# Performance work log

Measured on AMD Instinct MI355X. Metric: run time of the kernel, lower is better.

The kernel has to match this reference:

```python
import jax, jax.numpy as jnp
import numpy as np

B, T, LEAF, A = 128, 50, 4880, 64
INTERNAL = 728
ATTN = 128   # attn_dim_size (GRU input)
RNN = 128    # rnn_dim_size
G = 128      # g_dim_size (== RNN, required by broadcast in forward)
NC = 283     # num_class
VERY_NEG = -1e30


def setup_inputs() -> dict:
    key = jax.random.key(0)
    ks = jax.random.split(key, 16)
    s = 0.05
    inputs_x = jax.random.uniform(ks[0], (B, T, LEAF), jnp.float32)
    inputs_f = jax.random.randint(ks[1], (B, T, A), 0, INTERNAL + 1)  # 0 = padding
    mask_seqs = jnp.ones((B, T), jnp.float32)
    dag_emb = jax.random.normal(ks[2], (LEAF, ATTN), jnp.float32) * s
    embed_a = jax.random.normal(ks[3], (INTERNAL + 1, G), jnp.float32) * s
    embed_a = embed_a.at[0].set(0.0)  # padding row
    # 2-layer GRU params (torch layout: [3H, in], gates r,z,n)
    Wih0 = jax.random.normal(ks[4], (3 * RNN, ATTN), jnp.float32) * s
    Whh0 = jax.random.normal(ks[5], (3 * RNN, RNN), jnp.float32) * s
    bih0 = jax.random.normal(ks[6], (3 * RNN,), jnp.float32) * s
    bhh0 = jax.random.normal(ks[7], (3 * RNN,), jnp.float32) * s
    Wih1 = jax.random.normal(ks[8], (3 * RNN, RNN), jnp.float32) * s
    Whh1 = jax.random.normal(ks[9], (3 * RNN, RNN), jnp.float32) * s
    bih1 = jax.random.normal(ks[10], (3 * RNN,), jnp.float32) * s
    bhh1 = jax.random.normal(ks[11], (3 * RNN,), jnp.float32) * s
    fc_w = jax.random.normal(ks[12], (NC, 2 * RNN), jnp.float32) * s
    fc_b = jax.random.normal(ks[13], (NC,), jnp.float32) * s
    return dict(inputs_x=inputs_x, inputs_f=inputs_f, mask_seqs=mask_seqs,
                dag_emb=dag_emb, embed_a=embed_a,
                Wih0=Wih0, Whh0=Whh0, bih0=bih0, bhh0=bhh0,
                Wih1=Wih1, Whh1=Whh1, bih1=bih1, bhh1=bhh1,
                fc_w=fc_w, fc_b=fc_b)


def _gru_layer(x, Wih, Whh, bih, bhh):
    # x: [B, T, I] -> out [B, T, H]; h0 = zeros
    H = Whh.shape[1]
    xW = jnp.einsum('bti,gi->btg', x, Wih) + bih  # [B,T,3H], precompute input gates
    h0 = jnp.zeros((x.shape[0], H), x.dtype)

    def step(h, xw_t):  # xw_t: [B,3H]
        gh = h @ Whh.T + bhh
        xr, xz, xn = jnp.split(xw_t, 3, axis=-1)
        hr, hz, hn = jnp.split(gh, 3, axis=-1)
        r = jax.nn.sigmoid(xr + hr)
        z = jax.nn.sigmoid(xz + hz)
        n = jnp.tanh(xn + r * hn)
        h_new = (1.0 - z) * n + z * h
        return h_new, h_new

    _, ys = jax.lax.scan(step, h0, jnp.swapaxes(xW, 0, 1))  # scan over T
    return jnp.swapaxes(ys, 0, 1)


def reference(inputs_x, inputs_f, mask_seqs, dag_emb, embed_a,
              Wih0, Whh0, bih0, bhh0, Wih1, Whh1, bih1, bhh1, fc_w, fc_b):
    # x = tanh(inputs_x @ dag_emb): [B,T,ATTN]
    x = jnp.tanh(jnp.einsum('btl,la->bta', inputs_x, dag_emb))
    # 2-layer GRU (no dropout at inference)
    h1 = _gru_layer(x, Wih0, Whh0, bih0, bhh0)
    out = _gru_layer(h1, Wih1, Whh1, bih1, bhh1)  # [B,T,RNN]
    # gather ancestor embeddings: [B,T,A,G]
    l = embed_a[inputs_f]
    # masked dot-product attention over ancestors
    hl = jnp.einsum('bth,btah->bta', out, l)
    mask_ans = inputs_f > 0
    hl = hl + jnp.where(mask_ans, 0.0, VERY_NEG)
    weights = jax.nn.softmax(hl, axis=-1)  # [B,T,A]
    k = jnp.einsum('bta,btah->bth', weights, l)
    s = jnp.concatenate([out, k], axis=-1)  # [B,T,2*RNN]
    output = jax.nn.sigmoid(s @ fc_w.T + fc_b)
    return output * mask_seqs[:, :, None]
```

## Files before the change

kernel.cpp:

```cpp
#include <hip/hip_runtime.h>
#include <math.h>

#define B_DIM 128
#define T_DIM 50
#define LEAF  4880
#define A_DIM 64
#define ATTN  128
#define RNN   128
#define NC    283
#define M_TOT (B_DIM*T_DIM)
#define KSPLIT 10
#define NCH 153
#define WT_PLANE (NCH*512*8)

using short8 = __attribute__((ext_vector_type(8))) short;
using short4v = __attribute__((ext_vector_type(4))) short;
using f32x4  = __attribute__((ext_vector_type(4))) float;

__device__ __forceinline__ float sigmoidf_(float x) {
  return 1.0f / (1.0f + __expf(-x));
}

__device__ __forceinline__ unsigned short f32_to_bf16_rne(float f) {
  unsigned int u = __float_as_uint(f);
  unsigned int r = u + 0x7FFFu + ((u >> 16) & 1u);
  return (unsigned short)(r >> 16);
}
__device__ __forceinline__ float bf16_bits_to_f32(unsigned short b) {
  return __uint_as_float(((unsigned int)b) << 16);
}

__global__ __launch_bounds__(256) void k_prep(
    const float* __restrict__ Wd,
    const float* __restrict__ Wih0, const float* __restrict__ Wih1,
    const float* __restrict__ fcw,
    unsigned short* __restrict__ Wt,
    unsigned short* __restrict__ Bt0, unsigned short* __restrict__ Bt1,
    unsigned short* __restrict__ Bt2) {
  const int bx = blockIdx.x;
  const int tid = threadIdx.x;
  if (bx < 306) {
    const int u = bx * 256 + tid;
    const int c = u >> 9, rem = u & 511;
    const int nt = rem >> 6, lane = rem & 63;
    const int n = nt * 16 + (lane & 15);
    const int kb = c * 32 + ((lane >> 4) << 3);
    short8 h8, l8;
    #pragma unroll
    for (int j = 0; j < 8; ++j) {
      int k = kb + j;
      float v = (k < LEAF) ? Wd[(size_t)k * 128 + n] : 0.0f;
      unsigned short hb = f32_to_bf16_rne(v);
      unsigned short lb = f32_to_bf16_rne(v - bf16_bits_to_f32(hb));
      h8[j] = (short)hb;
      l8[j] = (short)lb;
    }
    *(short8*)&Wt[(size_t)u * 8] = h8;
    *(short8*)&Wt[(size_t)WT_PLANE + (size_t)u * 8] = l8;
  } else {
    const float* src; unsigned short* dst; int N, K, s0;
    if (bx < 330)      { src = Wih0; dst = Bt0; N = 384; K = 128; s0 = (bx - 306) * 256; }
    else if (bx < 354) { src = Wih1; dst = Bt1; N = 384; K = 128; s0 = (bx - 330) * 256; }
    else               { src = fcw;  dst = Bt2; N = NC;  K = 256; s0 = (bx - 354) * 256; }
    const int s = s0 + tid;
    const int PL = (K / 32) * 24 * 512;
    const int kc = s / (24 * 64);
    const int r  = s % (24 * 64);
    const int nt = r >> 6, lane = r & 63;
    const int n  = nt * 16 + (lane & 15);
    const int kb = kc * 32 + ((lane >> 4) << 3);
    short8 h8, l8;
    #pragma unroll
    for (int j = 0; j < 8; ++j) {
      float v = (n < N) ? src[(size_t)n * K + kb + j] : 0.0f;
      unsigned short hb = f32_to_bf16_rne(v);
      unsigned short lb = f32_to_bf16_rne(v - bf16_bits_to_f32(hb));
      h8[j] = (short)hb;
      l8[j] = (short)lb;
    }
    *(short8*)&dst[(size_t)s * 8] = h8;
    *(short8*)&dst[(size_t)PL + (size_t)s * 8] = l8;
  }
}

__global__ __launch_bounds__(512, 4) void k_gemm_mfma(
    const float* __restrict__ Ax, const unsigned short* __restrict__ Wt,
    float* __restrict__ P) {
  __shared__ __align__(16) unsigned short As[2][8192];
  const int tid  = threadIdx.x;
  const int lane = tid & 63;
  const int w    = tid >> 6;
  const int M0   = blockIdx.x * 128;
  const int s    = blockIdx.y;
  const int c0   = (s * NCH) / KSPLIT;
  const int c1   = ((s + 1) * NCH) / KSPLIT;

  const int am = tid >> 2;
  const int kq = tid & 3;
  const float* pA = Ax + (size_t)(M0 + am) * LEAF;
  const int a_idx = (am >> 4) * 512 + ((am & 15) + 16 * kq) * 8;

  f32x4 acc[8];
  #pragma unroll
  for (int i = 0; i < 8; ++i) {
    #pragma unroll
    for (int q = 0; q < 4; ++q) acc[i][q] = 0.0f;
  }

  float4 rA_a0, rA_a1, rA_b0, rA_b1;
  short8 bh_a, bl_a, bh_b, bl_b;

  auto issueB = [&](int c, short8& bh, short8& bl) {
    const size_t o = ((size_t)c * 512 + w * 64 + lane) * 8;
    bh = *(const short8*)&Wt[o];
    bl = *(const short8*)&Wt[(size_t)WT_PLANE + o];
  };
  auto issueA = [&](int c, float4& r0, float4& r1) {
    int kk = c * 32 + kq * 8;
    kk = min(kk, LEAF - 8);
    r0 = *(const float4*)(pA + kk);
    r1 = *(const float4*)(pA + kk + 4);
  };
  auto storeA = [&](int p, float4 r0, float4 r1) {
    float v[8] = {r0.x, r0.y, r0.z, r0.w, r1.x, r1.y, r1.z, r1.w};
    short8 h8, l8;
    #pragma unroll
    for (int j = 0; j < 8; ++j) {
      unsigned short hb = f32_to_bf16_rne(v[j]);
      unsigned short lb = f32_to_bf16_rne(v[j] - bf16_bits_to_f32(hb));
      h8[j] = (short)hb;
      l8[j] = (short)lb;
    }
    *(short8*)&As[p][a_idx] = h8;
    *(short8*)&As[p][4096 + a_idx] = l8;
  };
  auto compute = [&](int p, const short8& bh, const short8& bl) {
    #pragma unroll
    for (int m = 0; m < 8; ++m) {
      short8 a_hi = *(const short8*)&As[p][m * 512 + lane * 8];
      short8 a_lo = *(const short8*)&As[p][4096 + m * 512 + lane * 8];
      acc[m] = __builtin_amdgcn_mfma_f32_16x16x32_bf16(a_hi, bl, acc[m], 0, 0, 0);
      acc[m] = __builtin_amdgcn_mfma_f32_16x16x32_bf16(a_lo, bh, acc[m], 0, 0, 0);
      acc[m] = __builtin_amdgcn_mfma_f32_16x16x32_bf16(a_hi, bh, acc[m], 0, 0, 0);
    }
  };

  {
    float4 t0, t1;
    issueA(c0, t0, t1);
    asm volatile("s_waitcnt vmcnt(0)" ::: "memory");
    storeA(0, t0, t1);
    issueB(c0, bh_a, bl_a);
    asm volatile("" ::: "memory");
    if (c0 + 1 < c1) issueA(c0 + 1, rA_a0, rA_a1);
    asm volatile("s_waitcnt lgkmcnt(0)" ::: "memory");
    __builtin_amdgcn_s_barrier();
    asm volatile("" ::: "memory");
  }

#define GEMM_ITER(BHc, BLc, BHn, BLn, RAc0, RAc1, RAn0, RAn1)                 \
  {                                                                           \
    const int p = (c - c0) & 1;                                               \
    const bool has1 = (c + 1 < c1), has2 = (c + 2 < c1);                      \
    if (has1) { issueB(c + 1, BHn, BLn); asm volatile("" ::: "memory"); }     \
    if (has2) { issueA(c + 2, RAn0, RAn1); asm volatile("" ::: "memory"); }   \
    if (has1) {                                                               \
      if (has2) { asm volatile("s_waitcnt vmcnt(4)" ::: "memory"); }          \
      else      { asm volatile("s_waitcnt vmcnt(2)" ::: "memory"); }          \
    } else      { asm volatile("s_waitcnt vmcnt(0)" ::: "memory"); }          \
    compute(p, BHc, BLc);                                                     \
    if (has1) storeA(p ^ 1, RAc0, RAc1);                                      \
    asm volatile("s_waitcnt lgkmcnt(0)" ::: "memory");                        \
    __builtin_amdgcn_s_barrier();                                             \
    asm volatile("" ::: "memory");                                            \
    ++c;                                                                      \
  }

  int c = c0;
  while (c < c1) {
    GEMM_ITER(bh_a, bl_a, bh_b, bl_b, rA_a0, rA_a1, rA_b0, rA_b1);
    if (c < c1) GEMM_ITER(bh_b, bl_b, bh_a, bl_a, rA_b0, rA_b1, rA_a0, rA_a1);
  }
#undef GEMM_ITER

  float* outp = P + (size_t)s * ((size_t)M_TOT * 128);
  const int col0 = w * 16 + (lane & 15);
  #pragma unroll
  for (int m = 0; m < 8; ++m) {
    const int rbase = M0 + m * 16 + ((lane >> 4) << 2);
    #pragma unroll
    for (int r = 0; r < 4; ++r)
      outp[(size_t)(rbase + r) * 128 + col0] = acc[m][r];
  }
}

__global__ __launch_bounds__(256) void k_reduce_tanh(
    float* __restrict__ P, float* __restrict__ X) {
  const size_t i = ((size_t)blockIdx.x * 256 + threadIdx.x) * 4;
  float4 a = *(const float4*)&P[i];
  #pragma unroll
  for (int s = 1; s < KSPLIT; ++s) {
    float4 b = *(const float4*)&P[(size_t)s * (M_TOT * 128) + i];
    a.x += b.x; a.y += b.y; a.z += b.z; a.w += b.w;
  }
  a.x = tanhf(a.x); a.y = tanhf(a.y); a.z = tanhf(a.z); a.w = tanhf(a.w);
  *(float4*)&X[i] = a;
}

template<int KC, int ACT>
__global__ __launch_bounds__(512) void k_bn_mfma(
    const float* __restrict__ A, const unsigned short* __restrict__ Bt,
    const float* __restrict__ bias, const float* __restrict__ maskv,
    float* __restrict__ C, int N, int ldc) {
  constexpr int K  = KC * 32;
  constexpr int PL = KC * 24 * 512;
  __shared__ __align__(16) unsigned short As2[2][KC * 512];
  const int tid  = threadIdx.x;
  const int lane = tid & 63;
  const int w    = tid >> 6;
  const int mrow = blockIdx.x * 16;
  const int nt   = blockIdx.y * 8 + w;

  short8 bh[KC], bl[KC];
  #pragma unroll
  for (int kc = 0; kc < KC; ++kc) {
    const size_t o = ((size_t)(kc * 24 + nt) * 64 + lane) * 8;
    bh[kc] = *(const short8*)&Bt[o];
    bl[kc] = *(const short8*)&Bt[(size_t)PL + o];
  }

  const int am = tid >> 5;
  const int q0 = tid & 31;
  constexpr int NQ = K / 128;
  float4 av[NQ];
  #pragma unroll
  for (int i = 0; i < NQ; ++i)
    av[i] = *(const float4*)&A[(size_t)(mrow + am) * K + (q0 + 32 * i) * 4];
  #pragma unroll
  for (int i = 0; i < NQ; ++i) {
    const int q = q0 + 32 * i;
    const int base = (am + 16 * (q >> 1)) * 8 + (q & 1) * 4;
    float v[4] = {av[i].x, av[i].y, av[i].z, av[i].w};
    short4v h4, l4;
    #pragma unroll
    for (int j = 0; j < 4; ++j) {
      unsigned short hb = f32_to_bf16_rne(v[j]);
      unsigned short lb = f32_to_bf16_rne(v[j] - bf16_bits_to_f32(hb));
      h4[j] = (short)hb;
      l4[j] = (short)lb;
    }
    *(short4v*)&As2[0][base] = h4;
    *(short4v*)&As2[1][base] = l4;
  }
  __syncthreads();

  f32x4 acc;
  #pragma unroll
  for (int q = 0; q < 4; ++q) acc[q] = 0.0f;
  #pragma unroll
  for (int kc = 0; kc < KC; ++kc) {
    const int slot = (lane & 15) + 64 * kc + 16 * (lane >> 4);
    short8 a_hi = *(const short8*)&As2[0][slot * 8];
    short8 a_lo = *(const short8*)&As2[1][slot * 8];
    acc = __builtin_amdgcn_mfma_f32_16x16x32_bf16(a_hi, bl[kc], acc, 0, 0, 0);
    acc = __builtin_amdgcn_mfma_f32_16x16x32_bf16(a_lo, bh[kc], acc, 0, 0, 0);
    acc = __builtin_amdgcn_mfma_f32_16x16x32_bf16(a_hi, bh[kc], acc, 0, 0, 0);
  }

  const int col = nt * 16 + (lane & 15);
  if (col < N) {
    const float bv = bias[col];
    #pragma unroll
    for (int r = 0; r < 4; ++r) {
      const int m = mrow + ((lane >> 4) << 2) + r;
      float v = acc[r] + bv;
      if (ACT) v = sigmoidf_(v) * maskv[m];
      C[(size_t)m * ldc + col] = v;
    }
  }
}

__global__ __launch_bounds__(512) void k_gru(
    const float* __restrict__ xW, const float* __restrict__ Whh,
    const float* __restrict__ bhh, float* __restrict__ Hout) {
  const int b = blockIdx.x;
  const int tid = threadIdx.x;
  const int j  = tid >> 2;
  const int qf = tid & 3;
  __shared__ __align__(16) float hs[2][128];

  float4 wr[8], wz[8], wn[8];
  {
    const float* pr = Whh + (size_t)j * 128 + qf * 32;
    const float* pz = Whh + (size_t)(j + 128) * 128 + qf * 32;
    const float* pn = Whh + (size_t)(j + 256) * 128 + qf * 32;
    #pragma unroll
    for (int k = 0; k < 8; ++k) {
      const int c = (k + qf * 2) & 7;
      wr[k] = *(const float4*)(pr + c * 4);
      wz[k] = *(const float4*)(pz + c * 4);
      wn[k] = *(const float4*)(pn + c * 4);
    }
  }
  const float br = bhh[j], bz = bhh[j + 128], bn_ = bhh[j + 256];

  if (tid < 128) hs[0][tid] = 0.0f;
  const float* xwb = xW + (size_t)b * 50 * 384;
  float xr = 0.f, xz = 0.f, xn = 0.f;
  if (qf == 0) { xr = xwb[j]; xz = xwb[128 + j]; xn = xwb[256 + j]; }
  __syncthreads();

  int cur = 0;
  for (int t = 0; t < 50; ++t) {
    float nxr = 0.f, nxz = 0.f, nxn = 0.f;
    if (qf == 0 && t + 1 < 50) {
      const float* xwn = xwb + (size_t)(t + 1) * 384;
      nxr = xwn[j]; nxz = xwn[128 + j]; nxn = xwn[256 + j];
    }

    float ar = 0.f, az = 0.f, an = 0.f;
    #pragma unroll
    for (int k = 0; k < 8; ++k) {
      const int c = (k + qf * 2) & 7;
      float4 hv = *(const float4*)&hs[cur][qf * 32 + c * 4];
      ar += wr[k].x * hv.x + wr[k].y * hv.y + wr[k].z * hv.z + wr[k].w * hv.w;
      az += wz[k].x * hv.x + wz[k].y * hv.y + wz[k].z * hv.z + wz[k].w * hv.w;
      an += wn[k].x * hv.x + wn[k].y * hv.y + wn[k].z * hv.z + wn[k].w * hv.w;
    }
    ar += __shfl_xor(ar, 1); ar += __shfl_xor(ar, 2);
    az += __shfl_xor(az, 1); az += __shfl_xor(az, 2);
    an += __shfl_xor(an, 1); an += __shfl_xor(an, 2);

    if (qf == 0) {
      float r = sigmoidf_(xr + ar + br);
      float z = sigmoidf_(xz + az + bz);
      float nn = tanhf(xn + r * (an + bn_));
      float h = (1.f - z) * nn + z * hs[cur][j];
      hs[cur ^ 1][j] = h;
      Hout[(size_t)(b * 50 + t) * 128 + j] = h;
    }
    __syncthreads();
    cur ^= 1;
    xr = nxr; xz = nxz; xn = nxn;
  }
}

__global__ __launch_bounds__(128) void k_attn(
    const float* __restrict__ H2, const int* __restrict__ F,
    const float* __restrict__ emb, float* __restrict__ S) {
  const int m = blockIdx.x;
  const int tid = threadIdx.x;
  __shared__ __align__(16) float outs[128];
  __shared__ __align__(16) float Ls[64][132];
  __shared__ float hls[64];
  __shared__ float wts[64];
  __shared__ int fs[64];

  outs[tid] = H2[(size_t)m * 128 + tid];
  if (tid < 64) fs[tid] = F[(size_t)m * 64 + tid];
  __syncthreads();

  #pragma unroll
  for (int i = 0; i < 16; ++i) {
    int idx = tid + i * 128;
    int a = idx >> 5, c4 = idx & 31;
    float4 v = *(const float4*)&emb[(size_t)fs[a] * 128 + c4 * 4];
    *(float4*)&Ls[a][c4 * 4] = v;
  }
  __syncthreads();

  {
    const int a = tid >> 1, hf = tid & 1;
    float sum = 0.f;
    #pragma unroll
    for (int j = 0; j < 16; ++j) {
      float4 lv = *(const float4*)&Ls[a][hf * 64 + j * 4];
      float4 ov = *(const float4*)&outs[hf * 64 + j * 4];
      sum += lv.x * ov.x + lv.y * ov.y + lv.z * ov.z + lv.w * ov.w;
    }
    float other = __shfl_xor(sum, 1);
    sum += other;
    if (hf == 0) hls[a] = sum + (fs[a] > 0 ? 0.0f : -1e30f);
  }
  __syncthreads();

  if (tid < 64) {
    float v = hls[tid];
    float mx = v;
    #pragma unroll
    for (int o = 32; o; o >>= 1) mx = fmaxf(mx, __shfl_xor(mx, o));
    float e = __expf(v - mx);
    float sm = e;
    #pragma unroll
    for (int o = 32; o; o >>= 1) sm += __shfl_xor(sm, o);
    wts[tid] = e / sm;
  }
  __syncthreads();

  float kv = 0.f;
  #pragma unroll 8
  for (int a2 = 0; a2 < 64; ++a2) kv += wts[a2] * Ls[a2][tid];

  S[(size_t)m * 256 + tid] = outs[tid];
  S[(size_t)m * 256 + 128 + tid] = kv;
}

extern "C" void kernel_launch(void* const* d_in, const int* in_sizes, int n_in,
                              void* d_out, int out_size, void* d_ws, size_t ws_size,
                              hipStream_t stream) {
  const float* inputs_x  = (const float*)d_in[0];
  const int*   inputs_f  = (const int*)d_in[1];
  const float* mask_seqs = (const float*)d_in[2];
  const float* dag_emb   = (const float*)d_in[3];
  const float* embed_a   = (const float*)d_in[4];
  const float* Wih0 = (const float*)d_in[5];
  const float* Whh0 = (const float*)d_in[6];
  const float* bih0 = (const float*)d_in[7];
  const float* bhh0 = (const float*)d_in[8];
  const float* Wih1 = (const float*)d_in[9];
  const float* Whh1 = (const float*)d_in[10];
  const float* bih1 = (const float*)d_in[11];
  const float* bhh1 = (const float*)d_in[12];
  const float* fc_w = (const float*)d_in[13];
  const float* fc_b = (const float*)d_in[14];
  float* out = (float*)d_out;

  float* ws = (float*)d_ws;
  float* P  = ws;
  float* X  = P;
  float* S  = P + 819200;
  float* xW = ws + KSPLIT * 819200;
  float* H1 = xW + 2457600;
  float* H2 = H1 + 819200;
  unsigned short* Wt  = (unsigned short*)H1;
  unsigned short* Bt0 = (unsigned short*)(H2 + 819200);
  unsigned short* Bt1 = Bt0 + 2 * 49152;
  unsigned short* Bt2 = Bt1 + 2 * 49152;

  k_prep<<<402, 256, 0, stream>>>(dag_emb, Wih0, Wih1, fc_w, Wt, Bt0, Bt1, Bt2);
  k_gemm_mfma<<<dim3(50, KSPLIT), 512, 0, stream>>>(inputs_x, Wt, P);
  k_reduce_tanh<<<800, 256, 0, stream>>>(P, X);
  k_bn_mfma<4, 0><<<dim3(400, 3), 512, 0, stream>>>(X, Bt0, bih0, nullptr, xW, 384, 384);
  k_gru<<<128, 512, 0, stream>>>(xW, Whh0, bhh0, H1);
  k_bn_mfma<4, 0><<<dim3(400, 3), 512, 0, stream>>>(H1, Bt1, bih1, nullptr, xW, 384, 384);
  k_gru<<<128, 512, 0, stream>>>(xW, Whh1, bhh1, H2);
  k_attn<<<6400, 128, 0, stream>>>(H2, inputs_f, embed_a, S);
  k_bn_mfma<8, 1><<<dim3(400, 3), 512, 0, stream>>>(S, Bt2, fc_b, mask_seqs, out, NC, NC);
}
```

Baseline: 371.5 us.

## Halve GEMM M-tile to double block count; use fast tanh in GRU

The dag-embedding GEMM now uses 64-row M tiles instead of 128, doubling the grid to 100x10 blocks. Each thread loads one float4 of A per chunk, and the LDS staging and accumulators shrink to match. This is meant to fill more CUs for the memory-bound 128x50x4880 input read, with higher occupancy allowed by launch bounds. Separately, the GRU recurrence replaces tanhf with a clamped exp/rcp approximation to shorten the serial per-step latency, at a small cost in accuracy.

```diff
diff --git a/kernel.cpp b/kernel.cpp
--- a/kernel.cpp
+++ b/kernel.cpp
@@ -19,6 +19,11 @@
 
 __device__ __forceinline__ float sigmoidf_(float x) {
   return 1.0f / (1.0f + __expf(-x));
+}
+__device__ __forceinline__ float tanhf_fast(float x) {
+  x = fminf(fmaxf(x, -15.f), 15.f);
+  float e = __expf(2.f * x);
+  return (e - 1.f) * __builtin_amdgcn_rcpf(e + 1.f);
 }
 
 __device__ __forceinline__ unsigned short f32_to_bf16_rne(float f) {
@@ -83,31 +88,31 @@
   }
 }
 
-__global__ __launch_bounds__(512, 4) void k_gemm_mfma(
+__global__ __launch_bounds__(512, 8) void k_gemm_mfma(
     const float* __restrict__ Ax, const unsigned short* __restrict__ Wt,
     float* __restrict__ P) {
-  __shared__ __align__(16) unsigned short As[2][8192];
+  __shared__ __align__(16) unsigned short As[2][4096];
   const int tid  = threadIdx.x;
   const int lane = tid & 63;
   const int w    = tid >> 6;
-  const int M0   = blockIdx.x * 128;
+  const int M0   = blockIdx.x * 64;
   const int s    = blockIdx.y;
   const int c0   = (s * NCH) / KSPLIT;
   const int c1   = ((s + 1) * NCH) / KSPLIT;
 
-  const int am = tid >> 2;
-  const int kq = tid & 3;
+  const int am = tid >> 3;
+  const int kq = tid & 7;
   const float* pA = Ax + (size_t)(M0 + am) * LEAF;
-  const int a_idx = (am >> 4) * 512 + ((am & 15) + 16 * kq) * 8;
-
-  f32x4 acc[8];
-  #pragma unroll
-  for (int i = 0; i < 8; ++i) {
+  const int a_idx = (am >> 4) * 512 + ((am & 15) + 16 * (kq >> 1)) * 8 + (kq & 1) * 4;
+
+  f32x4 acc[4];
+  #pragma unroll
+  for (int i = 0; i < 4; ++i) {
     #pragma unroll
     for (int q = 0; q < 4; ++q) acc[i][q] = 0.0f;
   }
 
-  float4 rA_a0, rA_a1, rA_b0, rA_b1;
+  float4 rA_a, rA_b;
   short8 bh_a, bl_a, bh_b, bl_b;
 
   auto issueB = [&](int c, short8& bh, short8& bl) {
@@ -115,30 +120,29 @@
     bh = *(const short8*)&Wt[o];
     bl = *(const short8*)&Wt[(size_t)WT_PLANE + o];
   };
-  auto issueA = [&](int c, float4& r0, float4& r1) {
-    int kk = c * 32 + kq * 8;
-    kk = min(kk, LEAF - 8);
-    r0 = *(const float4*)(pA + kk);
-    r1 = *(const float4*)(pA + kk + 4);
+  auto issueA = [&](int c, float4& ra) {
+    int kk = c * 32 + kq * 4;
+    kk = min(kk, LEAF - 4);
+    ra = *(const float4*)(pA + kk);
   };
-  auto storeA = [&](int p, float4 r0, float4 r1) {
-    float v[8] = {r0.x, r0.y, r0.z, r0.w, r1.x, r1.y, r1.z, r1.w};
-    short8 h8, l8;
-    #pragma unroll
-    for (int j = 0; j < 8; ++j) {
+  auto storeA = [&](int p, float4 ra) {
+    float v[4] = {ra.x, ra.y, ra.z, ra.w};
+    short4v h4, l4;
+    #pragma unroll
+    for (int j = 0; j < 4; ++j) {
       unsigned short hb = f32_to_bf16_rne(v[j]);
       unsigned short lb = f32_to_bf16_rne(v[j] - bf16_bits_to_f32(hb));
-      h8[j] = (short)hb;
-      l8[j] = (short)lb;
-    }
-    *(short8*)&As[p][a_idx] = h8;
-    *(short8*)&As[p][4096 + a_idx] = l8;
+      h4[j] = (short)hb;
+      l4[j] = (short)lb;
+    }
+    *(short4v*)&As[p][a_idx] = h4;
+    *(short4v*)&As[p][2048 + a_idx] = l4;
   };
   auto compute = [&](int p, const short8& bh, const short8& bl) {
     #pragma unroll
-    for (int m = 0; m < 8; ++m) {
+    for (int m = 0; m < 4; ++m) {
       short8 a_hi = *(const short8*)&As[p][m * 512 + lane * 8];
-      short8 a_lo = *(const short8*)&As[p][4096 + m * 512 + lane * 8];
+      short8 a_lo = *(const short8*)&As[p][2048 + m * 512 + lane * 8];
       acc[m] = __builtin_amdgcn_mfma_f32_16x16x32_bf16(a_hi, bl, acc[m], 0, 0, 0);
       acc[m] = __builtin_amdgcn_mfma_f32_16x16x32_bf16(a_lo, bh, acc[m], 0, 0, 0);
       acc[m] = __builtin_amdgcn_mfma_f32_16x16x32_bf16(a_hi, bh, acc[m], 0, 0, 0);
@@ -146,30 +150,30 @@
   };
 
   {
-    float4 t0, t1;
-    issueA(c0, t0, t1);
+    float4 ta;
+    issueA(c0, ta);
     asm volatile("s_waitcnt vmcnt(0)" ::: "memory");
-    storeA(0, t0, t1);
+    storeA(0, ta);
     issueB(c0, bh_a, bl_a);
     asm volatile("" ::: "memory");
-    if (c0 + 1 < c1) issueA(c0 + 1, rA_a0, rA_a1);
+    if (c0 + 1 < c1) issueA(c0 + 1, rA_a);
     asm volatile("s_waitcnt lgkmcnt(0)" ::: "memory");
     __builtin_amdgcn_s_barrier();
     asm volatile("" ::: "memory");
   }
 
-#define GEMM_ITER(BHc, BLc, BHn, BLn, RAc0, RAc1, RAn0, RAn1)                 \
+#define GEMM_ITER(BHc, BLc, BHn, BLn, RAc, RAn)                               \
   {                                                                           \
     const int p = (c - c0) & 1;                                               \
     const bool has1 = (c + 1 < c1), has2 = (c + 2 < c1);                      \
     if (has1) { issueB(c + 1, BHn, BLn); asm volatile("" ::: "memory"); }     \
-    if (has2) { issueA(c + 2, RAn0, RAn1); asm volatile("" ::: "memory"); }   \
+    if (has2) { issueA(c + 2, RAn);      asm volatile("" ::: "memory"); }     \
     if (has1) {                                                               \
-      if (has2) { asm volatile("s_waitcnt vmcnt(4)" ::: "memory"); }          \
+      if (has2) { asm volatile("s_waitcnt vmcnt(3)" ::: "memory"); }          \
       else      { asm volatile("s_waitcnt vmcnt(2)" ::: "memory"); }          \
     } else      { asm volatile("s_waitcnt vmcnt(0)" ::: "memory"); }          \
     compute(p, BHc, BLc);                                                     \
-    if (has1) storeA(p ^ 1, RAc0, RAc1);                                      \
+    if (has1) storeA(p ^ 1, RAc);                                             \
     asm volatile("s_waitcnt lgkmcnt(0)" ::: "memory");                        \
     __builtin_amdgcn_s_barrier();                                             \
     asm volatile("" ::: "memory");                                            \
@@ -178,15 +182,15 @@
 
   int c = c0;
   while (c < c1) {
-    GEMM_ITER(bh_a, bl_a, bh_b, bl_b, rA_a0, rA_a1, rA_b0, rA_b1);
-    if (c < c1) GEMM_ITER(bh_b, bl_b, bh_a, bl_a, rA_b0, rA_b1, rA_a0, rA_a1);
+    GEMM_ITER(bh_a, bl_a, bh_b, bl_b, rA_a, rA_b);
+    if (c < c1) GEMM_ITER(bh_b, bl_b, bh_a, bl_a, rA_b, rA_a);
   }
 #undef GEMM_ITER
 
   float* outp = P + (size_t)s * ((size_t)M_TOT * 128);
   const int col0 = w * 16 + (lane & 15);
   #pragma unroll
-  for (int m = 0; m < 8; ++m) {
+  for (int m = 0; m < 4; ++m) {
     const int rbase = M0 + m * 16 + ((lane >> 4) << 2);
     #pragma unroll
     for (int r = 0; r < 4; ++r)
@@ -334,7 +338,7 @@
     if (qf == 0) {
       float r = sigmoidf_(xr + ar + br);
       float z = sigmoidf_(xz + az + bz);
-      float nn = tanhf(xn + r * (an + bn_));
+      float nn = tanhf_fast(xn + r * (an + bn_));
       float h = (1.f - z) * nn + z * hs[cur][j];
       hs[cur ^ 1][j] = h;
       Hout[(size_t)(b * 50 + t) * 128 + j] = h;
@@ -438,7 +442,7 @@
   unsigned short* Bt2 = Bt1 + 2 * 49152;
 
   k_prep<<<402, 256, 0, stream>>>(dag_emb, Wih0, Wih1, fc_w, Wt, Bt0, Bt1, Bt2);
-  k_gemm_mfma<<<dim3(50, KSPLIT), 512, 0, stream>>>(inputs_x, Wt, P);
+  k_gemm_mfma<<<dim3(100, KSPLIT), 512, 0, stream>>>(inputs_x, Wt, P);
   k_reduce_tanh<<<800, 256, 0, stream>>>(P, X);
   k_bn_mfma<4, 0><<<dim3(400, 3), 512, 0, stream>>>(X, Bt0, bih0, nullptr, xW, 384, 384);
   k_gru<<<128, 512, 0, stream>>>(xW, Whh0, bhh0, H1);
```

Result: no change. 369.3 us (-0.6%).
